# Optimization experiments

Hardware: AMD Instinct MI355X
Metric: run time of the kernel (lower is better)

The kernel has to match this reference:

```python
import jax, jax.numpy as jnp
import numpy as np

EPS = 1e-5
SLOPE = 0.2


def knn_feature(x, k):
    # x: (B,N,C) -> (B,N,k,2C) edge features: concat(neighbor - center, center)
    xx = jnp.sum(x * x, axis=-1)                      # (B,N)
    inner = jnp.einsum('bnc,bmc->bnm', x, x)          # (B,N,N)
    pair = 2.0 * inner - xx[:, :, None] - xx[:, None, :]  # negative squared dist
    idx = jax.lax.top_k(pair, k)[1]                   # (B,N,k) nearest neighbors
    nbr = jax.vmap(lambda xb, ib: xb[ib])(x, idx)     # (B,N,k,C) gather
    ctr = jnp.broadcast_to(x[:, :, None, :], nbr.shape)
    return jnp.concatenate([nbr - ctr, ctr], axis=-1)


def conv_bn_lrelu(h, w, g, b):
    # 1x1 conv == pointwise matmul; BN in training mode (batch stats, biased var)
    h = jnp.einsum('bnkc,oc->bnko', h, w)
    m = jnp.mean(h, axis=(0, 1, 2))
    v = jnp.mean(jnp.square(h - m), axis=(0, 1, 2))
    h = g * (h - m) * jax.lax.rsqrt(v + EPS) + b
    return jnp.where(h >= 0, h, SLOPE * h)


def setup_inputs() -> dict:
    key = jax.random.key(0)
    B, N, C, K, H, O = 4, 4096, 3, 20, 64, 64
    ks = jax.random.split(key, 10)
    x = jax.random.normal(ks[0], (B, N, C), dtype=jnp.float32)
    def w(kk, o, i):
        return jax.random.normal(kk, (o, i), dtype=jnp.float32) * (1.0 / np.sqrt(i))
    return {
        'x': x,
        'w1': w(ks[1], H, 2 * C),
        'w2': w(ks[2], H, H),
        'w3': w(ks[3], H, H),
        'w4': w(ks[4], H, 2 * H),
        'w5': w(ks[5], H, H),
        'w6': w(ks[6], H, H),
        'w7': w(ks[7], H, 2 * H),
        'w8': w(ks[8], H, H),
        'w9': w(ks[9], O, H),
        'gamma': jnp.ones((9, H), dtype=jnp.float32),
        'beta': jnp.zeros((9, H), dtype=jnp.float32),
        'k': 20,
    }


def reference(x, w1, w2, w3, w4, w5, w6, w7, w8, w9, gamma, beta, k):
    h = knn_feature(x, k)                      # (B,N,k,6)
    h = conv_bn_lrelu(h, w1, gamma[0], beta[0])
    h = conv_bn_lrelu(h, w2, gamma[1], beta[1])
    h = conv_bn_lrelu(h, w3, gamma[2], beta[2])
    x1 = jnp.max(h, axis=2)                    # (B,N,64)
    h = knn_feature(x1, k)                     # (B,N,k,128)
    h = conv_bn_lrelu(h, w4, gamma[3], beta[3])
    h = conv_bn_lrelu(h, w5, gamma[4], beta[4])
    h = conv_bn_lrelu(h, w6, gamma[5], beta[5])
    x2 = jnp.max(h, axis=2)                    # (B,N,64)
    h = knn_feature(x2, k)                     # (B,N,k,128)
    h = conv_bn_lrelu(h, w7, gamma[6], beta[6])
    h = conv_bn_lrelu(h, w8, gamma[7], beta[7])
    h = conv_bn_lrelu(h, w9, gamma[8], beta[8])
    x3 = jnp.max(h, axis=2)                    # (B,N,out_features)
    return x3
```

## Files before the change

kernel.cpp:

```cpp
#include <hip/hip_runtime.h>

namespace {

constexpr int Bc   = 4;
constexpr int Nc   = 4096;
constexpr int Kc   = 20;
constexpr int BNc  = Bc * Nc;
constexpr int PIXc = BNc * Kc;
constexpr float  NEGINF = -3.0e38f;
constexpr double EPSD   = (double)1e-5f;

template<int C>
__global__ __launch_bounds__(256)
void compute_xx_xla(const float* __restrict__ X, float* __restrict__ xxf) {
    int i = blockIdx.x * 256 + threadIdx.x;
    if (i >= BNc) return;
    const float* xp = X + (size_t)i * C;
    if constexpr (C == 3) {
        const float q0 = __fmul_rn(xp[0], xp[0]);
        const float q1 = __fmul_rn(xp[1], xp[1]);
        const float q2 = __fmul_rn(xp[2], xp[2]);
        xxf[i] = __fadd_rn(__fadd_rn(q0, q1), q2);
    } else {
        float acc[16];
#pragma unroll
        for (int l = 0; l < 16; ++l) acc[l] = 0.f;
#pragma unroll
        for (int blk = 0; blk < 4; ++blk)
#pragma unroll
            for (int l = 0; l < 16; ++l)
                acc[l] = __fadd_rn(acc[l], __fmul_rn(xp[blk * 16 + l], xp[blk * 16 + l]));
        float a8[8];
#pragma unroll
        for (int l = 0; l < 8; ++l) a8[l] = __fadd_rn(acc[l], acc[l + 8]);
        float a4[4];
#pragma unroll
        for (int l = 0; l < 4; ++l) a4[l] = __fadd_rn(a8[l], a8[l + 4]);
        xxf[i] = __fadd_rn(__fadd_rn(a4[0], a4[2]), __fadd_rn(a4[1], a4[3]));
    }
}

template<int C>
__global__ __launch_bounds__(256)
void pair_tile(const float* __restrict__ X, const float* __restrict__ xxf,
               float* __restrict__ S, int b) {
    constexpr int P = C + 1;
    __shared__ float sxn[64 * P], sxm[64 * P];
    __shared__ float sxxn[64], sxxm[64];
    const int tid = threadIdx.x;
    const int tn  = blockIdx.x >> 6;
    const int tm  = blockIdx.x & 63;
    const float* Xn = X + ((size_t)b * Nc + tn * 64) * C;
    const float* Xm = X + ((size_t)b * Nc + tm * 64) * C;
    for (int f = tid; f < 64 * C; f += 256) {
        const int row = f / C, c = f - row * C;
        sxn[row * P + c] = Xn[f];
        sxm[row * P + c] = Xm[f];
    }
    if (tid < 64)        sxxn[tid]      = xxf[b * Nc + tn * 64 + tid];
    else if (tid < 128)  sxxm[tid - 64] = xxf[b * Nc + tm * 64 + (tid - 64)];
    __syncthreads();

    const int rn0 = (tid >> 4) * 4;
    const int rm0 = (tid & 15) * 4;
    float a00=0,a01=0,a02=0,a03=0, a10=0,a11=0,a12=0,a13=0;
    float a20=0,a21=0,a22=0,a23=0, a30=0,a31=0,a32=0,a33=0;
#pragma unroll 4
    for (int c = 0; c < C; ++c) {
        const float n0 = sxn[(rn0    ) * P + c];
        const float n1 = sxn[(rn0 + 1) * P + c];
        const float n2 = sxn[(rn0 + 2) * P + c];
        const float n3 = sxn[(rn0 + 3) * P + c];
        const float m0 = sxm[(rm0    ) * P + c];
        const float m1 = sxm[(rm0 + 1) * P + c];
        const float m2 = sxm[(rm0 + 2) * P + c];
        const float m3 = sxm[(rm0 + 3) * P + c];
        a00 = __builtin_fmaf(n0, m0, a00); a01 = __builtin_fmaf(n0, m1, a01);
        a02 = __builtin_fmaf(n0, m2, a02); a03 = __builtin_fmaf(n0, m3, a03);
        a10 = __builtin_fmaf(n1, m0, a10); a11 = __builtin_fmaf(n1, m1, a11);
        a12 = __builtin_fmaf(n1, m2, a12); a13 = __builtin_fmaf(n1, m3, a13);
        a20 = __builtin_fmaf(n2, m0, a20); a21 = __builtin_fmaf(n2, m1, a21);
        a22 = __builtin_fmaf(n2, m2, a22); a23 = __builtin_fmaf(n2, m3, a23);
        a30 = __builtin_fmaf(n3, m0, a30); a31 = __builtin_fmaf(n3, m1, a31);
        a32 = __builtin_fmaf(n3, m2, a32); a33 = __builtin_fmaf(n3, m3, a33);
    }
    const float xm0 = sxxm[rm0], xm1 = sxxm[rm0 + 1], xm2 = sxxm[rm0 + 2], xm3 = sxxm[rm0 + 3];
#define PAIR_ROW(i, r0, r1, r2, r3)                                                     \
    {                                                                                   \
        const float xn_ = sxxn[rn0 + i];                                                \
        float4 v;                                                                       \
        v.x = __fsub_rn(__fsub_rn(__fmul_rn(2.0f, r0), xn_), xm0);                      \
        v.y = __fsub_rn(__fsub_rn(__fmul_rn(2.0f, r1), xn_), xm1);                      \
        v.z = __fsub_rn(__fsub_rn(__fmul_rn(2.0f, r2), xn_), xm2);                      \
        v.w = __fsub_rn(__fsub_rn(__fmul_rn(2.0f, r3), xn_), xm3);                      \
        *(float4*)&S[(size_t)(tn * 64 + rn0 + i) * Nc + tm * 64 + rm0] = v;             \
    }
    PAIR_ROW(0, a00, a01, a02, a03)
    PAIR_ROW(1, a10, a11, a12, a13)
    PAIR_ROW(2, a20, a21, a22, a23)
    PAIR_ROW(3, a30, a31, a32, a33)
#undef PAIR_ROW
}

__global__ __launch_bounds__(256)
void brute_select(const float* __restrict__ S, int* __restrict__ knnIdx, int b) {
    const int lane = threadIdx.x & 63;
    const int wv   = threadIdx.x >> 6;
    const int n    = blockIdx.x * 4 + wv;
    const float* Sr = S + (size_t)n * Nc;
    float v[64];
#pragma unroll
    for (int j = 0; j < 64; ++j) v[j] = Sr[j * 64 + lane];
    int* outp = knnIdx + ((size_t)b * Nc + n) * Kc;
    for (int round = 0; round < Kc; ++round) {
        float bv = NEGINF; int bi = 0x7fffffff;
#pragma unroll
        for (int j = 0; j < 64; ++j) {
            const int mi = j * 64 + lane;
            const bool better = (v[j] > bv) || (v[j] == bv && mi < bi);
            bv = better ? v[j] : bv;
            bi = better ? mi : bi;
        }
#pragma unroll
        for (int s = 1; s < 64; s <<= 1) {
            const float ov = __shfl_xor(bv, s);
            const int   oi = __shfl_xor(bi, s);
            const bool better = (ov > bv) || (ov == bv && oi < bi);
            bv = better ? ov : bv;
            bi = better ? oi : bi;
        }
        if (lane == 0) outp[round] = bi;
#pragma unroll
        for (int j = 0; j < 64; ++j)
            if (j == (bi >> 6) && (bi & 63) == lane) v[j] = NEGINF;
    }
}

__device__ __forceinline__ float bn_lrelu_np(float hv, float m, float r,
                                             float g, float bb) {
    float t = __fsub_rn(hv, m);
    t = __fmul_rn(g, t);
    t = __fmul_rn(t, r);
    t = __fadd_rn(t, bb);
    return t >= 0.f ? t : __fmul_rn(0.2f, t);
}

__global__ __launch_bounds__(256)
void edge_conv3(const float* __restrict__ X, const int* __restrict__ knn,
                const float* __restrict__ W, float* __restrict__ h,
                double* __restrict__ stats) {
    constexpr int F = 6, PW = 8, TP = 64;
    __shared__ float sA[TP * PW];
    __shared__ float sWT[F * 65];
    __shared__ double sp[4 * 128];
    const int tid = threadIdx.x;
    for (int f = tid; f < 64 * F; f += 256) {
        const int o = f / F, cc = f - o * F;
        sWT[cc * 65 + o] = W[f];
    }
    const int pix0 = blockIdx.x * TP;
    for (int f = tid; f < TP * F; f += 256) {
        const int pix = f / F, c = f - pix * F;
        const int p  = pix0 + pix;
        const int bn = p / Kc;
        const int b  = bn >> 12;
        const int j  = knn[p];
        float v;
        if (c < 3) v = __fsub_rn(X[((size_t)(b << 12) + j) * 3 + c],
                                 X[(size_t)bn * 3 + c]);
        else       v = X[(size_t)bn * 3 + (c - 3)];
        sA[pix * PW + c] = v;
    }
    __syncthreads();
    const int ty = tid >> 4, tx = tid & 15;
    const int p0 = ty * 4, o0 = tx * 4;
    float acc[4][4];
#pragma unroll
    for (int i = 0; i < 4; ++i)
#pragma unroll
        for (int j = 0; j < 4; ++j) acc[i][j] = 0.f;
#pragma unroll
    for (int c = 0; c < F; ++c) {
        float av[4], wv[4];
#pragma unroll
        for (int i = 0; i < 4; ++i) av[i] = sA[(p0 + i) * PW + c];
#pragma unroll
        for (int j = 0; j < 4; ++j) wv[j] = sWT[c * 65 + o0 + j];
#pragma unroll
        for (int i = 0; i < 4; ++i)
#pragma unroll
            for (int j = 0; j < 4; ++j)
                acc[i][j] = __builtin_fmaf(av[i], wv[j], acc[i][j]);
    }
#pragma unroll
    for (int i = 0; i < 4; ++i)
        *(float4*)&h[(size_t)(pix0 + p0 + i) * 64 + o0] =
            make_float4(acc[i][0], acc[i][1], acc[i][2], acc[i][3]);
    double s1[4], s2[4];
#pragma unroll
    for (int j = 0; j < 4; ++j) { s1[j] = 0.0; s2[j] = 0.0; }
#pragma unroll
    for (int i = 0; i < 4; ++i)
#pragma unroll
        for (int j = 0; j < 4; ++j) {
            const double d = (double)acc[i][j];
            s1[j] += d; s2[j] += d * d;
        }
#pragma unroll
    for (int mask = 16; mask <= 32; mask <<= 1)
#pragma unroll
        for (int j = 0; j < 4; ++j) {
            s1[j] += __shfl_xor(s1[j], mask);
            s2[j] += __shfl_xor(s2[j], mask);
        }
    if ((tid & 48) == 0) {
        const int w = tid >> 6;
#pragma unroll
        for (int j = 0; j < 4; ++j) {
            sp[w * 128 + o0 + j]      = s1[j];
            sp[w * 128 + 64 + o0 + j] = s2[j];
        }
    }
    __syncthreads();
    if (tid < 128)
        atomicAdd(&stats[tid], sp[tid] + sp[128 + tid] + sp[256 + tid] + sp[384 + tid]);
}

__global__ __launch_bounds__(256)
void edge_conv64(const float* __restrict__ X, const int* __restrict__ knn,
                 const float* __restrict__ W, float* __restrict__ h,
                 double* __restrict__ stats) {
    __shared__ alignas(16) float smem[64 * 129 + 64 * 68];
    float*  sA  = smem;
    float*  sWT = smem + 64 * 129;
    double* sp  = (double*)smem;
    const int tid = threadIdx.x;
    const int pix0 = blockIdx.x * 64;
    for (int f = tid; f < 8192; f += 256) {
        const int pix = f >> 7, c = f & 127;
        const int p  = pix0 + pix;
        const int bn = p / Kc;
        const int b  = bn >> 12;
        const int j  = knn[p];
        float v;
        if (c < 64) v = __fsub_rn(X[((size_t)(b << 12) + j) * 64 + c],
                                  X[(size_t)bn * 64 + c]);
        else        v = X[(size_t)bn * 64 + (c - 64)];
        sA[pix * 129 + c] = v;
    }
    const int og = tid & 7, pg = tid >> 3;
    const int p0 = pg * 2, o0 = og * 8;
    float acc[2][8];
#pragma unroll
    for (int i = 0; i < 2; ++i)
#pragma unroll
        for (int j = 0; j < 8; ++j) acc[i][j] = 0.f;
#pragma unroll
    for (int ph = 0; ph < 2; ++ph) {
        for (int f = tid; f < 4096; f += 256) {
            const int o = f >> 6, cc = f & 63;
            sWT[cc * 68 + o] = W[o * 128 + ph * 64 + cc];
        }
        __syncthreads();
#pragma unroll 2
        for (int cc = 0; cc < 64; ++cc) {
            const int c = ph * 64 + cc;
            const float4 w0 = *(const float4*)&sWT[cc * 68 + o0];
            const float4 w1 = *(const float4*)&sWT[cc * 68 + o0 + 4];
            const float a0 = sA[(p0    ) * 129 + c];
            const float a1 = sA[(p0 + 1) * 129 + c];
            acc[0][0] = __builtin_fmaf(a0, w0.x, acc[0][0]); acc[0][1] = __builtin_fmaf(a0, w0.y, acc[0][1]);
            acc[0][2] = __builtin_fmaf(a0, w0.z, acc[0][2]); acc[0][3] = __builtin_fmaf(a0, w0.w, acc[0][3]);
            acc[0][4] = __builtin_fmaf(a0, w1.x, acc[0][4]); acc[0][5] = __builtin_fmaf(a0, w1.y, acc[0][5]);
            acc[0][6] = __builtin_fmaf(a0, w1.z, acc[0][6]); acc[0][7] = __builtin_fmaf(a0, w1.w, acc[0][7]);
            acc[1][0] = __builtin_fmaf(a1, w0.x, acc[1][0]); acc[1][1] = __builtin_fmaf(a1, w0.y, acc[1][1]);
            acc[1][2] = __builtin_fmaf(a1, w0.z, acc[1][2]); acc[1][3] = __builtin_fmaf(a1, w0.w, acc[1][3]);
            acc[1][4] = __builtin_fmaf(a1, w1.x, acc[1][4]); acc[1][5] = __builtin_fmaf(a1, w1.y, acc[1][5]);
            acc[1][6] = __builtin_fmaf(a1, w1.z, acc[1][6]); acc[1][7] = __builtin_fmaf(a1, w1.w, acc[1][7]);
        }
        __syncthreads();
    }
#pragma unroll
    for (int i = 0; i < 2; ++i) {
        float* dst = &h[(size_t)(pix0 + p0 + i) * 64 + o0];
        *(float4*)dst       = make_float4(acc[i][0], acc[i][1], acc[i][2], acc[i][3]);
        *(float4*)(dst + 4) = make_float4(acc[i][4], acc[i][5], acc[i][6], acc[i][7]);
    }
    double s1[8], s2[8];
#pragma unroll
    for (int j = 0; j < 8; ++j) { s1[j] = 0.0; s2[j] = 0.0; }
#pragma unroll
    for (int i = 0; i < 2; ++i)
#pragma unroll
        for (int j = 0; j < 8; ++j) {
            const double d = (double)acc[i][j];
            s1[j] += d; s2[j] += d * d;
        }
#pragma unroll
    for (int mask = 8; mask <= 32; mask <<= 1)
#pragma unroll
        for (int j = 0; j < 8; ++j) {
            s1[j] += __shfl_xor(s1[j], mask);
            s2[j] += __shfl_xor(s2[j], mask);
        }
    __syncthreads();
    if ((tid & 56) == 0) {
        const int w = tid >> 6;
#pragma unroll
        for (int j = 0; j < 8; ++j) {
            sp[w * 128 + o0 + j]      = s1[j];
            sp[w * 128 + 64 + o0 + j] = s2[j];
        }
    }
    __syncthreads();
    if (tid < 128)
        atomicAdd(&stats[tid], sp[tid] + sp[128 + tid] + sp[256 + tid] + sp[384 + tid]);
}

__global__ __launch_bounds__(256)
void hidden_conv_tile(float* __restrict__ h, const float* __restrict__ W,
                      const float* __restrict__ mr, const float* __restrict__ g,
                      const float* __restrict__ bt, double* __restrict__ stats) {
    __shared__ alignas(16) float smem[128 * 65 + 64 * 68];
    float*  sA  = smem;
    float*  sWT = smem + 128 * 65;
    double* sp  = (double*)smem;
    const int tid = threadIdx.x;
    for (int f = tid; f < 4096; f += 256) {
        const int o = f >> 6, c = f & 63;
        sWT[c * 68 + o] = W[f];
    }
    const size_t pix0 = (size_t)blockIdx.x * 128;
    for (int f = tid; f < 8192; f += 256) {
        const int pix = f >> 6, c = f & 63;
        const float hv = h[(pix0 + pix) * 64 + c];
        sA[pix * 65 + c] = bn_lrelu_np(hv, mr[c], mr[64 + c], g[c], bt[c]);
    }
    __syncthreads();

    const int og = tid & 7, pg = tid >> 3;
    const int p0 = pg * 4, o0 = og * 8;
    float acc[4][8];
#pragma unroll
    for (int i = 0; i < 4; ++i)
#pragma unroll
        for (int j = 0; j < 8; ++j) acc[i][j] = 0.f;
#pragma unroll 2
    for (int c = 0; c < 64; ++c) {
        const float4 w0 = *(const float4*)&sWT[c * 68 + o0];
        const float4 w1 = *(const float4*)&sWT[c * 68 + o0 + 4];
        float av[4];
#pragma unroll
        for (int i = 0; i < 4; ++i) av[i] = sA[(p0 + i) * 65 + c];
#pragma unroll
        for (int i = 0; i < 4; ++i) {
            acc[i][0] = __builtin_fmaf(av[i], w0.x, acc[i][0]);
            acc[i][1] = __builtin_fmaf(av[i], w0.y, acc[i][1]);
            acc[i][2] = __builtin_fmaf(av[i], w0.z, acc[i][2]);
            acc[i][3] = __builtin_fmaf(av[i], w0.w, acc[i][3]);
            acc[i][4] = __builtin_fmaf(av[i], w1.x, acc[i][4]);
            acc[i][5] = __builtin_fmaf(av[i], w1.y, acc[i][5]);
            acc[i][6] = __builtin_fmaf(av[i], w1.z, acc[i][6]);
            acc[i][7] = __builtin_fmaf(av[i], w1.w, acc[i][7]);
        }
    }
#pragma unroll
    for (int i = 0; i < 4; ++i) {
        float* dst = &h[(pix0 + p0 + i) * 64 + o0];
        *(float4*)dst       = make_float4(acc[i][0], acc[i][1], acc[i][2], acc[i][3]);
        *(float4*)(dst + 4) = make_float4(acc[i][4], acc[i][5], acc[i][6], acc[i][7]);
    }
    double s1[8], s2[8];
#pragma unroll
    for (int j = 0; j < 8; ++j) { s1[j] = 0.0; s2[j] = 0.0; }
#pragma unroll
    for (int i = 0; i < 4; ++i)
#pragma unroll
        for (int j = 0; j < 8; ++j) {
            const double d = (double)acc[i][j];
            s1[j] += d; s2[j] += d * d;
        }
#pragma unroll
    for (int mask = 8; mask <= 32; mask <<= 1)
#pragma unroll
        for (int j = 0; j < 8; ++j) {
            s1[j] += __shfl_xor(s1[j], mask);
            s2[j] += __shfl_xor(s2[j], mask);
        }
    __syncthreads();
    if ((tid & 56) == 0) {
        const int w = tid >> 6;
#pragma unroll
        for (int j = 0; j < 8; ++j) {
            sp[w * 128 + o0 + j]      = s1[j];
            sp[w * 128 + 64 + o0 + j] = s2[j];
        }
    }
    __syncthreads();
    if (tid < 128)
        atomicAdd(&stats[tid], sp[tid] + sp[128 + tid] + sp[256 + tid] + sp[384 + tid]);
}

__global__ __launch_bounds__(256)
void maxk_np(const float* __restrict__ h, const float* __restrict__ mr,
             const float* __restrict__ g, const float* __restrict__ bt,
             float* __restrict__ out) {
    const int i  = blockIdx.x * 256 + threadIdx.x;
    const int o  = i & 63;
    const int bn = i >> 6;
    const float m = mr[o], r = mr[64 + o], gg = g[o], bb = bt[o];
    const float* hp = h + (size_t)bn * Kc * 64 + o;
    float mx = NEGINF;
#pragma unroll
    for (int k = 0; k < Kc; ++k) mx = fmaxf(mx, bn_lrelu_np(hp[k * 64], m, r, gg, bb));
    out[i] = mx;
}

__global__ void finalize_f(const double* __restrict__ stats, float* __restrict__ mr) {
    const int o = threadIdx.x;
    const double inv  = 1.0 / (double)PIXc;
    const double mean = stats[o] * inv;
    const double var  = stats[64 + o] * inv - mean * mean;
    mr[o]      = (float)mean;
    mr[64 + o] = (float)(1.0 / sqrt(var + EPSD));
}

}

extern "C" void kernel_launch(void* const* d_in, const int* in_sizes, int n_in,
                              void* d_out, int out_size, void* d_ws, size_t ws_size,
                              hipStream_t stream) {
    (void)in_sizes; (void)n_in; (void)out_size; (void)ws_size;
    const float* x     = (const float*)d_in[0];
    const float* w[9]  = {(const float*)d_in[1], (const float*)d_in[2], (const float*)d_in[3],
                          (const float*)d_in[4], (const float*)d_in[5], (const float*)d_in[6],
                          (const float*)d_in[7], (const float*)d_in[8], (const float*)d_in[9]};
    const float* gamma = (const float*)d_in[10];
    const float* beta  = (const float*)d_in[11];
    float* out = (float*)d_out;

    double* statsD = (double*)d_ws;
    float*  mr     = (float*)(statsD + 9 * 128);
    float*  xxf    = mr + 9 * 128;
    int*  knnIdx   = (int*)(xxf + BNc);
    float* x1      = (float*)(knnIdx + PIXc);
    float* x2      = x1 + (size_t)BNc * 64;
    float* h       = x2 + (size_t)BNc * 64;
    float* S       = h;

    hipMemsetAsync(statsD, 0, 9 * 128 * sizeof(double), stream);

    compute_xx_xla<3><<<64, 256, 0, stream>>>(x, xxf);
    for (int b = 0; b < Bc; ++b) {
        pair_tile<3><<<4096, 256, 0, stream>>>(x, xxf, S, b);
        brute_select<<<1024, 256, 0, stream>>>(S, knnIdx, b);
    }
    edge_conv3<<<PIXc / 64, 256, 0, stream>>>(x, knnIdx, w[0], h, statsD + 0 * 128);
    finalize_f<<<1, 64, 0, stream>>>(statsD + 0 * 128, mr + 0 * 128);
    hidden_conv_tile<<<PIXc / 128, 256, 0, stream>>>(h, w[1], mr + 0 * 128, gamma + 0 * 64, beta + 0 * 64, statsD + 1 * 128);
    finalize_f<<<1, 64, 0, stream>>>(statsD + 1 * 128, mr + 1 * 128);
    hidden_conv_tile<<<PIXc / 128, 256, 0, stream>>>(h, w[2], mr + 1 * 128, gamma + 1 * 64, beta + 1 * 64, statsD + 2 * 128);
    finalize_f<<<1, 64, 0, stream>>>(statsD + 2 * 128, mr + 2 * 128);
    maxk_np<<<4096, 256, 0, stream>>>(h, mr + 2 * 128, gamma + 2 * 64, beta + 2 * 64, x1);

    compute_xx_xla<64><<<64, 256, 0, stream>>>(x1, xxf);
    for (int b = 0; b < Bc; ++b) {
        pair_tile<64><<<4096, 256, 0, stream>>>(x1, xxf, S, b);
        brute_select<<<1024, 256, 0, stream>>>(S, knnIdx, b);
    }
    edge_conv64<<<PIXc / 64, 256, 0, stream>>>(x1, knnIdx, w[3], h, statsD + 3 * 128);
    finalize_f<<<1, 64, 0, stream>>>(statsD + 3 * 128, mr + 3 * 128);
    hidden_conv_tile<<<PIXc / 128, 256, 0, stream>>>(h, w[4], mr + 3 * 128, gamma + 3 * 64, beta + 3 * 64, statsD + 4 * 128);
    finalize_f<<<1, 64, 0, stream>>>(statsD + 4 * 128, mr + 4 * 128);
    hidden_conv_tile<<<PIXc / 128, 256, 0, stream>>>(h, w[5], mr + 4 * 128, gamma + 4 * 64, beta + 4 * 64, statsD + 5 * 128);
    finalize_f<<<1, 64, 0, stream>>>(statsD + 5 * 128, mr + 5 * 128);
    maxk_np<<<4096, 256, 0, stream>>>(h, mr + 5 * 128, gamma + 5 * 64, beta + 5 * 64, x2);

    compute_xx_xla<64><<<64, 256, 0, stream>>>(x2, xxf);
    for (int b = 0; b < Bc; ++b) {
        pair_tile<64><<<4096, 256, 0, stream>>>(x2, xxf, S, b);
        brute_select<<<1024, 256, 0, stream>>>(S, knnIdx, b);
    }
    edge_conv64<<<PIXc / 64, 256, 0, stream>>>(x2, knnIdx, w[6], h, statsD + 6 * 128);
    finalize_f<<<1, 64, 0, stream>>>(statsD + 6 * 128, mr + 6 * 128);
    hidden_conv_tile<<<PIXc / 128, 256, 0, stream>>>(h, w[7], mr + 6 * 128, gamma + 6 * 64, beta + 6 * 64, statsD + 7 * 128);
    finalize_f<<<1, 64, 0, stream>>>(statsD + 7 * 128, mr + 7 * 128);
    hidden_conv_tile<<<PIXc / 128, 256, 0, stream>>>(h, w[8], mr + 7 * 128, gamma + 7 * 64, beta + 7 * 64, statsD + 8 * 128);
    finalize_f<<<1, 64, 0, stream>>>(statsD + 8 * 128, mr + 8 * 128);
    maxk_np<<<4096, 256, 0, stream>>>(h, mr + 8 * 128, gamma + 8 * 64, beta + 8 * 64, out);
}
```

Baseline: 3.426 ms.

## Fuse pairwise distance and top-k selection into one streaming kNN kernel

Replaces the per-batch pair_tile plus brute_select launches, which write and re-read a full N x N distance matrix through global memory, with one kernel per layer. Each block owns 64 query rows, streams candidate tiles through shared memory, and keeps per-thread top-20 lists in registers. The four partial lists per row are then merged by a single thread. This removes the large global S traffic and eight launches per kNN stage. In exchange only 256 blocks run, the loop over the 64 candidate tiles is serial within each block, and the final merge is single-threaded per row, so parallelism and occupancy are lower.

```diff
diff --git a/kernel.cpp b/kernel.cpp
--- a/kernel.cpp
+++ b/kernel.cpp
@@ -42,97 +42,129 @@
 
 template<int C>
 __global__ __launch_bounds__(256)
-void pair_tile(const float* __restrict__ X, const float* __restrict__ xxf,
-               float* __restrict__ S, int b) {
+void knn_fused(const float* __restrict__ X, const float* __restrict__ xxf,
+               int* __restrict__ knnIdx) {
     constexpr int P = C + 1;
-    __shared__ float sxn[64 * P], sxm[64 * P];
-    __shared__ float sxxn[64], sxxm[64];
+    constexpr int CMPF = 2 * 64 * P + 64 * 65 + 128;
+    constexpr int MRGB = 64 * 80 * 8;
+    constexpr int SMEMB = (CMPF * 4 > MRGB) ? CMPF * 4 : MRGB;
+    __shared__ alignas(16) char smem_raw[SMEMB];
+    float* sxn   = (float*)smem_raw;
+    float* sxm   = sxn + 64 * P;
+    float* Sb    = sxm + 64 * P;
+    float* sxxn  = Sb + 64 * 65;
+    float* sxxm  = sxxn + 64;
+    float* candV = (float*)smem_raw;
+    int*   candI = (int*)(candV + 64 * 80);
+
     const int tid = threadIdx.x;
-    const int tn  = blockIdx.x >> 6;
-    const int tm  = blockIdx.x & 63;
+    const int b   = blockIdx.x >> 6;
+    const int tn  = blockIdx.x & 63;
+
     const float* Xn = X + ((size_t)b * Nc + tn * 64) * C;
-    const float* Xm = X + ((size_t)b * Nc + tm * 64) * C;
     for (int f = tid; f < 64 * C; f += 256) {
         const int row = f / C, c = f - row * C;
         sxn[row * P + c] = Xn[f];
-        sxm[row * P + c] = Xm[f];
-    }
-    if (tid < 64)        sxxn[tid]      = xxf[b * Nc + tn * 64 + tid];
-    else if (tid < 128)  sxxm[tid - 64] = xxf[b * Nc + tm * 64 + (tid - 64)];
-    __syncthreads();
-
-    const int rn0 = (tid >> 4) * 4;
-    const int rm0 = (tid & 15) * 4;
-    float a00=0,a01=0,a02=0,a03=0, a10=0,a11=0,a12=0,a13=0;
-    float a20=0,a21=0,a22=0,a23=0, a30=0,a31=0,a32=0,a33=0;
+    }
+    if (tid < 64) sxxn[tid] = xxf[b * Nc + tn * 64 + tid];
+
+    float vals[Kc]; int idxs[Kc];
+#pragma unroll
+    for (int j = 0; j < Kc; ++j) { vals[j] = NEGINF; idxs[j] = -1; }
+    float mv = NEGINF;
+    const int selr = tid & 63, selc = tid >> 6;
+
+    const int ty = tid >> 4, tx = tid & 15;
+    const int rn0 = ty * 4, rm0 = tx * 4;
+
+    for (int tm = 0; tm < 64; ++tm) {
+        __syncthreads();
+        const float* Xm = X + ((size_t)b * Nc + tm * 64) * C;
+        for (int f = tid; f < 64 * C; f += 256) {
+            const int row = f / C, c = f - row * C;
+            sxm[row * P + c] = Xm[f];
+        }
+        if (tid < 64) sxxm[tid] = xxf[b * Nc + tm * 64 + tid];
+        __syncthreads();
+
+        float a[4][4];
+#pragma unroll
+        for (int i = 0; i < 4; ++i)
+#pragma unroll
+            for (int j = 0; j < 4; ++j) a[i][j] = 0.f;
 #pragma unroll 4
-    for (int c = 0; c < C; ++c) {
-        const float n0 = sxn[(rn0    ) * P + c];
-        const float n1 = sxn[(rn0 + 1) * P + c];
-        const float n2 = sxn[(rn0 + 2) * P + c];
-        const float n3 = sxn[(rn0 + 3) * P + c];
-        const float m0 = sxm[(rm0    ) * P + c];
-        const float m1 = sxm[(rm0 + 1) * P + c];
-        const float m2 = sxm[(rm0 + 2) * P + c];
-        const float m3 = sxm[(rm0 + 3) * P + c];
-        a00 = __builtin_fmaf(n0, m0, a00); a01 = __builtin_fmaf(n0, m1, a01);
-        a02 = __builtin_fmaf(n0, m2, a02); a03 = __builtin_fmaf(n0, m3, a03);
-        a10 = __builtin_fmaf(n1, m0, a10); a11 = __builtin_fmaf(n1, m1, a11);
-        a12 = __builtin_fmaf(n1, m2, a12); a13 = __builtin_fmaf(n1, m3, a13);
-        a20 = __builtin_fmaf(n2, m0, a20); a21 = __builtin_fmaf(n2, m1, a21);
-        a22 = __builtin_fmaf(n2, m2, a22); a23 = __builtin_fmaf(n2, m3, a23);
-        a30 = __builtin_fmaf(n3, m0, a30); a31 = __builtin_fmaf(n3, m1, a31);
-        a32 = __builtin_fmaf(n3, m2, a32); a33 = __builtin_fmaf(n3, m3, a33);
-    }
-    const float xm0 = sxxm[rm0], xm1 = sxxm[rm0 + 1], xm2 = sxxm[rm0 + 2], xm3 = sxxm[rm0 + 3];
-#define PAIR_ROW(i, r0, r1, r2, r3)                                                     \
-    {                                                                                   \
-        const float xn_ = sxxn[rn0 + i];                                                \
-        float4 v;                                                                       \
-        v.x = __fsub_rn(__fsub_rn(__fmul_rn(2.0f, r0), xn_), xm0);                      \
-        v.y = __fsub_rn(__fsub_rn(__fmul_rn(2.0f, r1), xn_), xm1);                      \
-        v.z = __fsub_rn(__fsub_rn(__fmul_rn(2.0f, r2), xn_), xm2);                      \
-        v.w = __fsub_rn(__fsub_rn(__fmul_rn(2.0f, r3), xn_), xm3);                      \
-        *(float4*)&S[(size_t)(tn * 64 + rn0 + i) * Nc + tm * 64 + rm0] = v;             \
-    }
-    PAIR_ROW(0, a00, a01, a02, a03)
-    PAIR_ROW(1, a10, a11, a12, a13)
-    PAIR_ROW(2, a20, a21, a22, a23)
-    PAIR_ROW(3, a30, a31, a32, a33)
-#undef PAIR_ROW
-}
-
-__global__ __launch_bounds__(256)
-void brute_select(const float* __restrict__ S, int* __restrict__ knnIdx, int b) {
-    const int lane = threadIdx.x & 63;
-    const int wv   = threadIdx.x >> 6;
-    const int n    = blockIdx.x * 4 + wv;
-    const float* Sr = S + (size_t)n * Nc;
-    float v[64];
-#pragma unroll
-    for (int j = 0; j < 64; ++j) v[j] = Sr[j * 64 + lane];
-    int* outp = knnIdx + ((size_t)b * Nc + n) * Kc;
-    for (int round = 0; round < Kc; ++round) {
-        float bv = NEGINF; int bi = 0x7fffffff;
-#pragma unroll
-        for (int j = 0; j < 64; ++j) {
-            const int mi = j * 64 + lane;
-            const bool better = (v[j] > bv) || (v[j] == bv && mi < bi);
-            bv = better ? v[j] : bv;
-            bi = better ? mi : bi;
-        }
-#pragma unroll
-        for (int s = 1; s < 64; s <<= 1) {
-            const float ov = __shfl_xor(bv, s);
-            const int   oi = __shfl_xor(bi, s);
-            const bool better = (ov > bv) || (ov == bv && oi < bi);
-            bv = better ? ov : bv;
-            bi = better ? oi : bi;
-        }
-        if (lane == 0) outp[round] = bi;
-#pragma unroll
-        for (int j = 0; j < 64; ++j)
-            if (j == (bi >> 6) && (bi & 63) == lane) v[j] = NEGINF;
+        for (int c = 0; c < C; ++c) {
+            float nv[4], mvv[4];
+#pragma unroll
+            for (int i = 0; i < 4; ++i) nv[i]  = sxn[(rn0 + i) * P + c];
+#pragma unroll
+            for (int j = 0; j < 4; ++j) mvv[j] = sxm[(rm0 + j) * P + c];
+#pragma unroll
+            for (int i = 0; i < 4; ++i)
+#pragma unroll
+                for (int j = 0; j < 4; ++j)
+                    a[i][j] = __builtin_fmaf(nv[i], mvv[j], a[i][j]);
+        }
+#pragma unroll
+        for (int i = 0; i < 4; ++i) {
+            const float xn_ = sxxn[rn0 + i];
+#pragma unroll
+            for (int j = 0; j < 4; ++j)
+                Sb[(rn0 + i) * 65 + rm0 + j] =
+                    __fsub_rn(__fsub_rn(__fmul_rn(2.0f, a[i][j]), xn_), sxxm[rm0 + j]);
+        }
+        __syncthreads();
+
+        const float* Srow = &Sb[selr * 65];
+        const int mbase = tm * 64;
+#pragma unroll
+        for (int i = 0; i < 16; ++i) {
+            const int mloc = i * 4 + selc;
+            const float val = Srow[mloc];
+            if (val > mv) {
+                const int m = mbase + mloc;
+                int slot = 0; int worst = -2;
+#pragma unroll
+                for (int j = 0; j < Kc; ++j) {
+                    const bool cnd = (vals[j] == mv) && (idxs[j] > worst);
+                    worst = cnd ? idxs[j] : worst;
+                    slot  = cnd ? j : slot;
+                }
+#pragma unroll
+                for (int j = 0; j < Kc; ++j) {
+                    vals[j] = (j == slot) ? val : vals[j];
+                    idxs[j] = (j == slot) ? m   : idxs[j];
+                }
+                float nm = 3.0e38f;
+#pragma unroll
+                for (int j = 0; j < Kc; ++j) nm = fminf(nm, vals[j]);
+                mv = nm;
+            }
+        }
+    }
+    __syncthreads();
+#pragma unroll
+    for (int s = 0; s < Kc; ++s) {
+        candV[selr * 80 + selc * Kc + s] = vals[s];
+        candI[selr * 80 + selc * Kc + s] = idxs[s];
+    }
+    __syncthreads();
+    if (tid < 64) {
+        const int r = tid;
+        int* outp = knnIdx + ((size_t)b * Nc + tn * 64 + r) * Kc;
+        for (int round = 0; round < Kc; ++round) {
+            float bv = NEGINF; int bi = 0x7fffffff; int bq = 0;
+            for (int q = 0; q < 80; ++q) {
+                const float v = candV[r * 80 + q];
+                const int   ii = candI[r * 80 + q];
+                const bool better = (v > bv) || (v == bv && ii < bi);
+                bv = better ? v : bv;
+                bi = better ? ii : bi;
+                bq = better ? q : bq;
+            }
+            outp[round] = bi;
+            candV[r * 80 + bq] = NEGINF;
+        }
     }
 }
 
@@ -446,15 +478,11 @@
     float* x1      = (float*)(knnIdx + PIXc);
     float* x2      = x1 + (size_t)BNc * 64;
     float* h       = x2 + (size_t)BNc * 64;
-    float* S       = h;
 
     hipMemsetAsync(statsD, 0, 9 * 128 * sizeof(double), stream);
 
     compute_xx_xla<3><<<64, 256, 0, stream>>>(x, xxf);
-    for (int b = 0; b < Bc; ++b) {
-        pair_tile<3><<<4096, 256, 0, stream>>>(x, xxf, S, b);
-        brute_select<<<1024, 256, 0, stream>>>(S, knnIdx, b);
-    }
+    knn_fused<3><<<256, 256, 0, stream>>>(x, xxf, knnIdx);
     edge_conv3<<<PIXc / 64, 256, 0, stream>>>(x, knnIdx, w[0], h, statsD + 0 * 128);
     finalize_f<<<1, 64, 0, stream>>>(statsD + 0 * 128, mr + 0 * 128);
     hidden_conv_tile<<<PIXc / 128, 256, 0, stream>>>(h, w[1], mr + 0 * 128, gamma + 0 * 64, beta + 0 * 64, statsD + 1 * 128);
@@ -464,10 +492,7 @@
     maxk_np<<<4096, 256, 0, stream>>>(h, mr + 2 * 128, gamma + 2 * 64, beta + 2 * 64, x1);
 
     compute_xx_xla<64><<<64, 256, 0, stream>>>(x1, xxf);
-    for (int b = 0; b < Bc; ++b) {
-        pair_tile<64><<<4096, 256, 0, stream>>>(x1, xxf, S, b);
-        brute_select<<<1024, 256, 0, stream>>>(S, knnIdx, b);
-    }
+    knn_fused<64><<<256, 256, 0, stream>>>(x1, xxf, knnIdx);
     edge_conv64<<<PIXc / 64, 256, 0, stream>>>(x1, knnIdx, w[3], h, statsD + 3 * 128);
     finalize_f<<<1, 64, 0, stream>>>(statsD + 3 * 128, mr + 3 * 128);
     hidden_conv_tile<<<PIXc / 128, 256, 0, stream>>>(h, w[4], mr + 3 * 128, gamma + 3 * 64, beta + 3 * 64, statsD + 4 * 128);
@@ -477,10 +502,7 @@
     maxk_np<<<4096, 256, 0, stream>>>(h, mr + 5 * 128, gamma + 5 * 64, beta + 5 * 64, x2);
 
     compute_xx_xla<64><<<64, 256, 0, stream>>>(x2, xxf);
-    for (int b = 0; b < Bc; ++b) {
-        pair_tile<64><<<4096, 256, 0, stream>>>(x2, xxf, S, b);
-        brute_select<<<1024, 256, 0, stream>>>(S, knnIdx, b);
-    }
+    knn_fused<64><<<256, 256, 0, stream>>>(x2, xxf, knnIdx);
     edge_conv64<<<PIXc / 64, 256, 0, stream>>>(x2, knnIdx, w[6], h, statsD + 6 * 128);
     finalize_f<<<1, 64, 0, stream>>>(statsD + 6 * 128, mr + 6 * 128);
     hidden_conv_tile<<<PIXc / 128, 256, 0, stream>>>(h, w[7], mr + 6 * 128, gamma + 6 * 64, beta + 6 * 64, statsD + 7 * 128);
```

New measurement: 3.900 ms. 13.8% more time.
